# Performance work log

Hardware: AMD Instinct MI355X
Metric: run time of the kernel (lower is better)

Reference implementation:

```python
import jax, jax.numpy as jnp
import numpy as np

NUM_SEGMENTS = 16

def setup_inputs() -> dict:
    key = jax.random.key(0)
    k1, k2, k3, k4 = jax.random.split(key, 4)
    C, R = 256, 4
    x = jax.random.normal(k1, (1000000, C), dtype=jnp.float32)
    indices = jax.random.randint(k2, (1000000,), 0, NUM_SEGMENTS, dtype=jnp.int64)
    # Linear weights (torch Linear: y = x @ W.T); store as (in, out) for einsum
    w1 = jax.random.normal(k3, (C, C // R), dtype=jnp.float32) / np.sqrt(C)
    w2 = jax.random.normal(k4, (C // R, C), dtype=jnp.float32) / np.sqrt(C // R)
    return {"x": x, "indices": indices, "w1": w1, "w2": w2}

def reference(x, indices, w1, w2):
    idx = indices.astype(jnp.int32)
    # scatter-mean over segments: (S, C)
    seg_sum = jax.ops.segment_sum(x, idx, num_segments=NUM_SEGMENTS)
    counts = jax.ops.segment_sum(jnp.ones((x.shape[0],), x.dtype), idx, num_segments=NUM_SEGMENTS)
    seg_mean = seg_sum / jnp.maximum(counts, 1.0)[:, None]
    # tiny SE MLP: Linear -> ReLU -> Linear -> Sigmoid
    h = jax.nn.relu(seg_mean @ w1)
    gate = jax.nn.sigmoid(h @ w2)  # (S, C)
    # gather per-point gate and modulate
    return x * gate[idx]
```

## Files before the change

### kernel.cpp

```cpp
#include <hip/hip_runtime.h>
#include <math.h>

#define C 256
#define S 16
#define CR 64
#define NREP 8

__global__ __launch_bounds__(128) void k_segsum(
    const float* __restrict__ x, const int* __restrict__ idx,
    float* __restrict__ psum, int* __restrict__ pcnt, int nrows)
{
    __shared__ float ls[S][C];
    __shared__ int   lc[S];
    const int t = threadIdx.x;

    #pragma unroll
    for (int i = t; i < S * C; i += 128) (&ls[0][0])[i] = 0.0f;
    if (t < S) lc[t] = 0;
    __syncthreads();

    const float2* __restrict__ x2 = reinterpret_cast<const float2*>(x);
    for (int row = blockIdx.x; row < nrows; row += gridDim.x) {
        const int s = idx[row];
        float2 v = x2[row * (C / 2) + t];
        float2* p = reinterpret_cast<float2*>(&ls[s][2 * t]);
        float2 cur = *p;
        cur.x += v.x; cur.y += v.y;
        *p = cur;
        if (t == 0) lc[s]++;
    }
    __syncthreads();

    const int rep = blockIdx.x & (NREP - 1);
    float* gs = psum + rep * S * C;
    int*   gc = pcnt + rep * S;
    for (int i = t; i < S * C; i += 128) atomicAdd(&gs[i], (&ls[0][0])[i]);
    if (t < S) atomicAdd(&gc[t], lc[t]);
}

__global__ __launch_bounds__(256) void k_mlp(
    const float* __restrict__ psum, const int* __restrict__ pcnt,
    const float* __restrict__ w1, const float* __restrict__ w2,
    float* __restrict__ gate)
{
    __shared__ float sm[S][C];
    __shared__ float h[S][CR];
    __shared__ float cnt[S];
    const int t = threadIdx.x;

    if (t < S) {
        int c = 0;
        #pragma unroll
        for (int r = 0; r < NREP; r++) c += pcnt[r * S + t];
        cnt[t] = fmaxf((float)c, 1.0f);
    }
    __syncthreads();

    for (int i = t; i < S * C; i += 256) {
        float v = 0.0f;
        #pragma unroll
        for (int r = 0; r < NREP; r++) v += psum[r * S * C + i];
        sm[i / C][i % C] = v / cnt[i / C];
    }
    __syncthreads();

    for (int o = t; o < S * CR; o += 256) {
        const int s = o / CR, j = o % CR;
        float acc = 0.0f;
        #pragma unroll 4
        for (int k = 0; k < C; k++) acc += sm[s][k] * w1[k * CR + j];
        h[s][j] = fmaxf(acc, 0.0f);
    }
    __syncthreads();

    for (int o = t; o < S * C; o += 256) {
        const int s = o / C, j = o % C;
        float acc = 0.0f;
        #pragma unroll
        for (int k = 0; k < CR; k++) acc += h[s][k] * w2[k * C + j];
        gate[o] = 1.0f / (1.0f + expf(-acc));
    }
}

__global__ __launch_bounds__(256) void k_mod(
    const float* __restrict__ x, const int* __restrict__ idx,
    const float* __restrict__ gate, float* __restrict__ out, int nrows)
{
    const int l    = threadIdx.x & 63;
    const int wrow = threadIdx.x >> 6;
    const float4* __restrict__ x4 = reinterpret_cast<const float4*>(x);
    const float4* __restrict__ g4 = reinterpret_cast<const float4*>(gate);
    float4* __restrict__ o4 = reinterpret_cast<float4*>(out);

    for (int row = blockIdx.x * 4 + wrow; row < nrows; row += gridDim.x * 4) {
        const int s = idx[row];
        float4 v = x4[row * (C / 4) + l];
        const float4 g = g4[s * (C / 4) + l];
        v.x *= g.x; v.y *= g.y; v.z *= g.z; v.w *= g.w;
        o4[row * (C / 4) + l] = v;
    }
}

extern "C" void kernel_launch(void* const* d_in, const int* in_sizes, int n_in,
                              void* d_out, int out_size, void* d_ws, size_t ws_size,
                              hipStream_t stream)
{
    const float* x   = (const float*)d_in[0];
    const int*   idx = (const int*)  d_in[1];
    const float* w1  = (const float*)d_in[2];
    const float* w2  = (const float*)d_in[3];
    float* out = (float*)d_out;
    const int nrows = in_sizes[1];

    float* psum = (float*)d_ws;
    int*   pcnt = (int*)(psum + NREP * S * C);
    float* gate = (float*)(pcnt + NREP * S);

    const size_t zero_bytes = NREP * S * C * sizeof(float) + NREP * S * sizeof(int);
    hipMemsetAsync(d_ws, 0, zero_bytes, stream);

    k_segsum<<<2048, 128, 0, stream>>>(x, idx, psum, pcnt, nrows);
    k_mlp<<<1, 256, 0, stream>>>(psum, pcnt, w1, w2, gate);
    k_mod<<<2048, 256, 0, stream>>>(x, idx, gate, out, nrows);
}
```

Baseline: 768.5 us.

## Accumulate segment sums in per-wave registers with software prefetch

The segment-sum kernel now gives each 64-lane wave its own rows and keeps all 16 segment accumulators as float4 registers. A wave-uniform switch selects which accumulator a row goes into, replacing the shared-memory read-modify-write and the block-level syncs. Loads are double-buffered two rows ahead to hide memory latency, and the flush uses more replicas (NREP=16) to spread atomic contention. The modulate kernel processes two rows per iteration to raise memory-level parallelism. The cost is much higher register pressure (64+ accumulator VGPRs) and more global atomics at the end.

```diff
diff --git a/kernel.cpp b/kernel.cpp
--- a/kernel.cpp
+++ b/kernel.cpp
@@ -4,38 +4,67 @@
 #define C 256
 #define S 16
 #define CR 64
-#define NREP 8
+#define NREP 16
 
-__global__ __launch_bounds__(128) void k_segsum(
+__global__ __launch_bounds__(256) void k_segsum(
     const float* __restrict__ x, const int* __restrict__ idx,
     float* __restrict__ psum, int* __restrict__ pcnt, int nrows)
 {
-    __shared__ float ls[S][C];
-    __shared__ int   lc[S];
-    const int t = threadIdx.x;
+    const int lane = threadIdx.x & 63;
+    const int wid  = __builtin_amdgcn_readfirstlane(
+                        (blockIdx.x * blockDim.x + threadIdx.x) >> 6);
+    const int nw   = (gridDim.x * blockDim.x) >> 6;
 
-    #pragma unroll
-    for (int i = t; i < S * C; i += 128) (&ls[0][0])[i] = 0.0f;
-    if (t < S) lc[t] = 0;
-    __syncthreads();
+    float4 a0={0,0,0,0},a1={0,0,0,0},a2={0,0,0,0},a3={0,0,0,0},
+           a4={0,0,0,0},a5={0,0,0,0},a6={0,0,0,0},a7={0,0,0,0},
+           a8={0,0,0,0},a9={0,0,0,0},a10={0,0,0,0},a11={0,0,0,0},
+           a12={0,0,0,0},a13={0,0,0,0},a14={0,0,0,0},a15={0,0,0,0};
+    int c0=0,c1=0,c2=0,c3=0,c4=0,c5=0,c6=0,c7=0,
+        c8=0,c9=0,c10=0,c11=0,c12=0,c13=0,c14=0,c15=0;
 
-    const float2* __restrict__ x2 = reinterpret_cast<const float2*>(x);
-    for (int row = blockIdx.x; row < nrows; row += gridDim.x) {
-        const int s = idx[row];
-        float2 v = x2[row * (C / 2) + t];
-        float2* p = reinterpret_cast<float2*>(&ls[s][2 * t]);
-        float2 cur = *p;
-        cur.x += v.x; cur.y += v.y;
-        *p = cur;
-        if (t == 0) lc[s]++;
+    const float4* __restrict__ x4 = reinterpret_cast<const float4*>(x);
+
+    int   row = wid;
+    bool  p0 = row < nrows;
+    float4 v0 = {0,0,0,0}; int s0 = 0;
+    if (p0) { v0 = x4[row * (C/4) + lane]; s0 = idx[row]; }
+    int   rowN = row + nw;
+    bool  p1 = rowN < nrows;
+    float4 v1 = {0,0,0,0}; int s1 = 0;
+    if (p1) { v1 = x4[rowN * (C/4) + lane]; s1 = idx[rowN]; }
+
+    while (p0) {
+        const int rowP = rowN + nw;
+        const bool p2 = rowP < nrows;
+        float4 v2 = {0,0,0,0}; int s2 = 0;
+        if (p2) { v2 = x4[rowP * (C/4) + lane]; s2 = idx[rowP]; }
+
+        #define ACASE(K) case K: a##K.x+=v0.x; a##K.y+=v0.y; a##K.z+=v0.z; a##K.w+=v0.w; c##K++; break;
+        switch (__builtin_amdgcn_readfirstlane(s0)) {
+            ACASE(0)  ACASE(1)  ACASE(2)  ACASE(3)
+            ACASE(4)  ACASE(5)  ACASE(6)  ACASE(7)
+            ACASE(8)  ACASE(9)  ACASE(10) ACASE(11)
+            ACASE(12) ACASE(13) ACASE(14) ACASE(15)
+        }
+        #undef ACASE
+
+        v0 = v1; s0 = s1; p0 = p1;
+        v1 = v2; s1 = s2; p1 = p2;
+        rowN = rowP;
     }
-    __syncthreads();
 
-    const int rep = blockIdx.x & (NREP - 1);
+    const int rep = wid & (NREP - 1);
     float* gs = psum + rep * S * C;
     int*   gc = pcnt + rep * S;
-    for (int i = t; i < S * C; i += 128) atomicAdd(&gs[i], (&ls[0][0])[i]);
-    if (t < S) atomicAdd(&gc[t], lc[t]);
+    #define FLUSH(K) { float* p = gs + K * C + 4 * lane; \
+        atomicAdd(p + 0, a##K.x); atomicAdd(p + 1, a##K.y); \
+        atomicAdd(p + 2, a##K.z); atomicAdd(p + 3, a##K.w); \
+        if (lane == 0 && c##K) atomicAdd(&gc[K], c##K); }
+    FLUSH(0)  FLUSH(1)  FLUSH(2)  FLUSH(3)
+    FLUSH(4)  FLUSH(5)  FLUSH(6)  FLUSH(7)
+    FLUSH(8)  FLUSH(9)  FLUSH(10) FLUSH(11)
+    FLUSH(12) FLUSH(13) FLUSH(14) FLUSH(15)
+    #undef FLUSH
 }
 
 __global__ __launch_bounds__(256) void k_mlp(
@@ -86,18 +115,31 @@
     const float* __restrict__ x, const int* __restrict__ idx,
     const float* __restrict__ gate, float* __restrict__ out, int nrows)
 {
-    const int l    = threadIdx.x & 63;
-    const int wrow = threadIdx.x >> 6;
+    const int l  = threadIdx.x & 63;
+    const int w  = threadIdx.x >> 6;
+    const int gw = blockIdx.x * 4 + w;
+    const int nw = gridDim.x * 4;
     const float4* __restrict__ x4 = reinterpret_cast<const float4*>(x);
     const float4* __restrict__ g4 = reinterpret_cast<const float4*>(gate);
     float4* __restrict__ o4 = reinterpret_cast<float4*>(out);
 
-    for (int row = blockIdx.x * 4 + wrow; row < nrows; row += gridDim.x * 4) {
-        const int s = idx[row];
-        float4 v = x4[row * (C / 4) + l];
-        const float4 g = g4[s * (C / 4) + l];
-        v.x *= g.x; v.y *= g.y; v.z *= g.z; v.w *= g.w;
-        o4[row * (C / 4) + l] = v;
+    for (int row = gw; row < nrows; row += 2 * nw) {
+        const int r2 = row + nw;
+        const bool has2 = r2 < nrows;
+        const int sA = idx[row];
+        float4 vA = x4[row * (C/4) + l];
+        int sB = 0; float4 vB = {0,0,0,0};
+        if (has2) { sB = idx[r2]; vB = x4[r2 * (C/4) + l]; }
+
+        const float4 gA = g4[sA * (C/4) + l];
+        vA.x *= gA.x; vA.y *= gA.y; vA.z *= gA.z; vA.w *= gA.w;
+        o4[row * (C/4) + l] = vA;
+
+        if (has2) {
+            const float4 gB = g4[sB * (C/4) + l];
+            vB.x *= gB.x; vB.y *= gB.y; vB.z *= gB.z; vB.w *= gB.w;
+            o4[r2 * (C/4) + l] = vB;
+        }
     }
 }
 
@@ -119,7 +161,7 @@
     const size_t zero_bytes = NREP * S * C * sizeof(float) + NREP * S * sizeof(int);
     hipMemsetAsync(d_ws, 0, zero_bytes, stream);
 
-    k_segsum<<<2048, 128, 0, stream>>>(x, idx, psum, pcnt, nrows);
+    k_segsum<<<1024, 256, 0, stream>>>(x, idx, psum, pcnt, nrows);
     k_mlp<<<1, 256, 0, stream>>>(psum, pcnt, w1, w2, gate);
     k_mod<<<2048, 256, 0, stream>>>(x, idx, gate, out, nrows);
 }
```

Result: slower. 940.8 us (+22.4%).

## Accumulate segment sums in per-wave registers instead of shared memory

Applied to the files above, without the earlier changes.

Rewrites the segment-sum kernel so each 64-lane wave processes 64-row superblocks. It keeps 16 float4 per-segment accumulators in registers, selected via a readlane-uniform switch, and computes counts with ballot/popcount. This removes the shared-memory read-modify-write per row and the block barriers, and loads float4 per lane with 4-row unrolled loads. In exchange, every wave flushes 16×256 atomics to global memory (NREP raised to 16), which adds heavy register pressure and many more global atomics.

```diff
diff --git a/kernel.cpp b/kernel.cpp
--- a/kernel.cpp
+++ b/kernel.cpp
@@ -4,38 +4,84 @@
 #define C 256
 #define S 16
 #define CR 64
-#define NREP 8
+#define NREP 16
 
-__global__ __launch_bounds__(128) void k_segsum(
+__global__ __launch_bounds__(256) void k_segsum(
     const float* __restrict__ x, const int* __restrict__ idx,
     float* __restrict__ psum, int* __restrict__ pcnt, int nrows)
 {
-    __shared__ float ls[S][C];
-    __shared__ int   lc[S];
-    const int t = threadIdx.x;
+    const int lane = threadIdx.x & 63;
+    const int wid  = (blockIdx.x * blockDim.x + threadIdx.x) >> 6;
+    const int nw   = (gridDim.x * blockDim.x) >> 6;
 
-    #pragma unroll
-    for (int i = t; i < S * C; i += 128) (&ls[0][0])[i] = 0.0f;
-    if (t < S) lc[t] = 0;
-    __syncthreads();
+    float4 a0={0,0,0,0},a1={0,0,0,0},a2={0,0,0,0},a3={0,0,0,0},
+           a4={0,0,0,0},a5={0,0,0,0},a6={0,0,0,0},a7={0,0,0,0},
+           a8={0,0,0,0},a9={0,0,0,0},a10={0,0,0,0},a11={0,0,0,0},
+           a12={0,0,0,0},a13={0,0,0,0},a14={0,0,0,0},a15={0,0,0,0};
+    int c0=0,c1=0,c2=0,c3=0,c4=0,c5=0,c6=0,c7=0,
+        c8=0,c9=0,c10=0,c11=0,c12=0,c13=0,c14=0,c15=0;
 
-    const float2* __restrict__ x2 = reinterpret_cast<const float2*>(x);
-    for (int row = blockIdx.x; row < nrows; row += gridDim.x) {
-        const int s = idx[row];
-        float2 v = x2[row * (C / 2) + t];
-        float2* p = reinterpret_cast<float2*>(&ls[s][2 * t]);
-        float2 cur = *p;
-        cur.x += v.x; cur.y += v.y;
-        *p = cur;
-        if (t == 0) lc[s]++;
+    const float4* __restrict__ x4 = reinterpret_cast<const float4*>(x);
+    const int nsb = nrows >> 6;
+
+    #define SCASE(K, V) case K: a##K.x+=V.x; a##K.y+=V.y; a##K.z+=V.z; a##K.w+=V.w; break;
+    #define SW(sv, V) switch (sv) { \
+        SCASE(0,V)  SCASE(1,V)  SCASE(2,V)  SCASE(3,V) \
+        SCASE(4,V)  SCASE(5,V)  SCASE(6,V)  SCASE(7,V) \
+        SCASE(8,V)  SCASE(9,V)  SCASE(10,V) SCASE(11,V) \
+        SCASE(12,V) SCASE(13,V) SCASE(14,V) SCASE(15,V) }
+
+    for (int sb = wid; sb < nsb; sb += nw) {
+        const int row0 = sb << 6;
+        const int vidx = idx[row0 + lane];
+        #define CNT(K) c##K += (int)__popcll(__ballot(vidx == K));
+        CNT(0)  CNT(1)  CNT(2)  CNT(3)  CNT(4)  CNT(5)  CNT(6)  CNT(7)
+        CNT(8)  CNT(9)  CNT(10) CNT(11) CNT(12) CNT(13) CNT(14) CNT(15)
+        #undef CNT
+
+        const float4* __restrict__ p = x4 + (size_t)row0 * (C/4) + lane;
+        for (int j = 0; j < 64; j += 4) {
+            const float4 v0 = p[(j+0) * (C/4)];
+            const float4 v1 = p[(j+1) * (C/4)];
+            const float4 v2 = p[(j+2) * (C/4)];
+            const float4 v3 = p[(j+3) * (C/4)];
+            const int s0 = __builtin_amdgcn_readlane(vidx, j+0);
+            const int s1 = __builtin_amdgcn_readlane(vidx, j+1);
+            const int s2 = __builtin_amdgcn_readlane(vidx, j+2);
+            const int s3 = __builtin_amdgcn_readlane(vidx, j+3);
+            SW(s0, v0) SW(s1, v1) SW(s2, v2) SW(s3, v3)
+        }
     }
-    __syncthreads();
 
-    const int rep = blockIdx.x & (NREP - 1);
+    if (wid == 0) {
+        #define TCASE(K, V) case K: a##K.x+=V.x; a##K.y+=V.y; a##K.z+=V.z; a##K.w+=V.w; c##K++; break;
+        for (int row = nsb << 6; row < nrows; ++row) {
+            const int s = idx[row];
+            const float4 v = x4[(size_t)row * (C/4) + lane];
+            switch (s) {
+                TCASE(0,v)  TCASE(1,v)  TCASE(2,v)  TCASE(3,v)
+                TCASE(4,v)  TCASE(5,v)  TCASE(6,v)  TCASE(7,v)
+                TCASE(8,v)  TCASE(9,v)  TCASE(10,v) TCASE(11,v)
+                TCASE(12,v) TCASE(13,v) TCASE(14,v) TCASE(15,v)
+            }
+        }
+        #undef TCASE
+    }
+    #undef SW
+    #undef SCASE
+
+    const int rep = wid & (NREP - 1);
     float* gs = psum + rep * S * C;
     int*   gc = pcnt + rep * S;
-    for (int i = t; i < S * C; i += 128) atomicAdd(&gs[i], (&ls[0][0])[i]);
-    if (t < S) atomicAdd(&gc[t], lc[t]);
+    #define FLUSH(K) { float* fp = gs + K * C + 4 * lane; \
+        atomicAdd(fp + 0, a##K.x); atomicAdd(fp + 1, a##K.y); \
+        atomicAdd(fp + 2, a##K.z); atomicAdd(fp + 3, a##K.w); \
+        if (lane == 0 && c##K) atomicAdd(&gc[K], c##K); }
+    FLUSH(0)  FLUSH(1)  FLUSH(2)  FLUSH(3)
+    FLUSH(4)  FLUSH(5)  FLUSH(6)  FLUSH(7)
+    FLUSH(8)  FLUSH(9)  FLUSH(10) FLUSH(11)
+    FLUSH(12) FLUSH(13) FLUSH(14) FLUSH(15)
+    #undef FLUSH
 }
 
 __global__ __launch_bounds__(256) void k_mlp(
@@ -119,7 +165,7 @@
     const size_t zero_bytes = NREP * S * C * sizeof(float) + NREP * S * sizeof(int);
     hipMemsetAsync(d_ws, 0, zero_bytes, stream);
 
-    k_segsum<<<2048, 128, 0, stream>>>(x, idx, psum, pcnt, nrows);
+    k_segsum<<<2048, 256, 0, stream>>>(x, idx, psum, pcnt, nrows);
     k_mlp<<<1, 256, 0, stream>>>(psum, pcnt, w1, w2, gate);
     k_mod<<<2048, 256, 0, stream>>>(x, idx, gate, out, nrows);
 }
```

Result: slower. 1.155 ms (+50.3%).

## Accumulate segment sums in per-wave registers and split counts into ballot histogram kernel

Applied to the files above, without the earlier changes.

The segment-sum kernel now keeps all 16 segment accumulators in registers per wavefront. Each row is added to every accumulator through a 0/1 multiply mask, which replaces the LDS read-modify-write done per row. Segment counts move to a separate ballot/popcount histogram kernel, and the replica count rises to 16. The intent is to remove LDS latency and serialization in the streaming pass, which reads 1 GB of x. The cost is 16x redundant FMAs per element, heavy register use, and one extra kernel launch.

```diff
diff --git a/kernel.cpp b/kernel.cpp
--- a/kernel.cpp
+++ b/kernel.cpp
@@ -4,38 +4,99 @@
 #define C 256
 #define S 16
 #define CR 64
-#define NREP 8
+#define NREP 16
 
-__global__ __launch_bounds__(128) void k_segsum(
+__global__ __launch_bounds__(256) void k_hist(
+    const int* __restrict__ idx, int* __restrict__ pcnt, int nrows)
+{
+    const int lane = threadIdx.x & 63;
+    const int tid  = blockIdx.x * blockDim.x + threadIdx.x;
+    const int T    = gridDim.x * blockDim.x;
+    const int padded = ((nrows + 63) >> 6) << 6;
+
+    int c0=0,c1=0,c2=0,c3=0,c4=0,c5=0,c6=0,c7=0,
+        c8=0,c9=0,c10=0,c11=0,c12=0,c13=0,c14=0,c15=0;
+
+    for (int i = tid; i < padded; i += T) {
+        const int v = (i < nrows) ? idx[i] : -1;
+        #define CNT(K) c##K += (int)__popcll(__ballot(v == K));
+        CNT(0)  CNT(1)  CNT(2)  CNT(3)  CNT(4)  CNT(5)  CNT(6)  CNT(7)
+        CNT(8)  CNT(9)  CNT(10) CNT(11) CNT(12) CNT(13) CNT(14) CNT(15)
+        #undef CNT
+    }
+    if (lane == 0) {
+        #define FL(K) if (c##K) atomicAdd(&pcnt[K], c##K);
+        FL(0)  FL(1)  FL(2)  FL(3)  FL(4)  FL(5)  FL(6)  FL(7)
+        FL(8)  FL(9)  FL(10) FL(11) FL(12) FL(13) FL(14) FL(15)
+        #undef FL
+    }
+}
+
+__global__ __launch_bounds__(256, 2) void k_segsum(
     const float* __restrict__ x, const int* __restrict__ idx,
-    float* __restrict__ psum, int* __restrict__ pcnt, int nrows)
+    float* __restrict__ psum, int nrows)
 {
-    __shared__ float ls[S][C];
-    __shared__ int   lc[S];
-    const int t = threadIdx.x;
+    const int lane = threadIdx.x & 63;
+    const int w    = threadIdx.x >> 6;
+    const int gw   = blockIdx.x * 4 + w;
+    const int nw   = gridDim.x * 4;
 
-    #pragma unroll
-    for (int i = t; i < S * C; i += 128) (&ls[0][0])[i] = 0.0f;
-    if (t < S) lc[t] = 0;
+    float4 a0={0,0,0,0},a1={0,0,0,0},a2={0,0,0,0},a3={0,0,0,0},
+           a4={0,0,0,0},a5={0,0,0,0},a6={0,0,0,0},a7={0,0,0,0},
+           a8={0,0,0,0},a9={0,0,0,0},a10={0,0,0,0},a11={0,0,0,0},
+           a12={0,0,0,0},a13={0,0,0,0},a14={0,0,0,0},a15={0,0,0,0};
+
+    const float4* __restrict__ x4 = reinterpret_cast<const float4*>(x);
+
+    #define ACC1(K, sv, vv) { const float m = (sv == K) ? 1.0f : 0.0f; \
+        a##K.x = fmaf(m, vv.x, a##K.x); a##K.y = fmaf(m, vv.y, a##K.y); \
+        a##K.z = fmaf(m, vv.z, a##K.z); a##K.w = fmaf(m, vv.w, a##K.w); }
+    #define ROW(sv, vv) \
+        ACC1(0,sv,vv)  ACC1(1,sv,vv)  ACC1(2,sv,vv)  ACC1(3,sv,vv) \
+        ACC1(4,sv,vv)  ACC1(5,sv,vv)  ACC1(6,sv,vv)  ACC1(7,sv,vv) \
+        ACC1(8,sv,vv)  ACC1(9,sv,vv)  ACC1(10,sv,vv) ACC1(11,sv,vv) \
+        ACC1(12,sv,vv) ACC1(13,sv,vv) ACC1(14,sv,vv) ACC1(15,sv,vv)
+
+    const int nbatch = nrows >> 2;
+    for (int b = gw; b < nbatch; b += nw) {
+        const int r = b << 2;
+        const int s0 = __builtin_amdgcn_readfirstlane(idx[r + 0]);
+        const int s1 = __builtin_amdgcn_readfirstlane(idx[r + 1]);
+        const int s2 = __builtin_amdgcn_readfirstlane(idx[r + 2]);
+        const int s3 = __builtin_amdgcn_readfirstlane(idx[r + 3]);
+        const float4* __restrict__ p = x4 + (size_t)r * (C/4) + lane;
+        const float4 v0 = p[0 * (C/4)];
+        const float4 v1 = p[1 * (C/4)];
+        const float4 v2 = p[2 * (C/4)];
+        const float4 v3 = p[3 * (C/4)];
+        ROW(s0, v0) ROW(s1, v1) ROW(s2, v2) ROW(s3, v3)
+    }
+    if (gw == 0) {
+        for (int r = nbatch << 2; r < nrows; ++r) {
+            const int s = __builtin_amdgcn_readfirstlane(idx[r]);
+            const float4 v = x4[(size_t)r * (C/4) + lane];
+            ROW(s, v)
+        }
+    }
+    #undef ROW
+    #undef ACC1
+
+    __shared__ float red[4][S][C];
+    #define ST(K) *reinterpret_cast<float4*>(&red[w][K][4 * lane]) = a##K;
+    ST(0)  ST(1)  ST(2)  ST(3)  ST(4)  ST(5)  ST(6)  ST(7)
+    ST(8)  ST(9)  ST(10) ST(11) ST(12) ST(13) ST(14) ST(15)
+    #undef ST
     __syncthreads();
 
-    const float2* __restrict__ x2 = reinterpret_cast<const float2*>(x);
-    for (int row = blockIdx.x; row < nrows; row += gridDim.x) {
-        const int s = idx[row];
-        float2 v = x2[row * (C / 2) + t];
-        float2* p = reinterpret_cast<float2*>(&ls[s][2 * t]);
-        float2 cur = *p;
-        cur.x += v.x; cur.y += v.y;
-        *p = cur;
-        if (t == 0) lc[s]++;
+    const int t   = threadIdx.x;
+    const int rep = blockIdx.x & (NREP - 1);
+    float* gs = psum + (size_t)rep * S * C;
+    #pragma unroll
+    for (int s_ = 0; s_ < S; s_++) {
+        const float v = red[0][s_][t] + red[1][s_][t] +
+                        red[2][s_][t] + red[3][s_][t];
+        atomicAdd(&gs[s_ * C + t], v);
     }
-    __syncthreads();
-
-    const int rep = blockIdx.x & (NREP - 1);
-    float* gs = psum + rep * S * C;
-    int*   gc = pcnt + rep * S;
-    for (int i = t; i < S * C; i += 128) atomicAdd(&gs[i], (&ls[0][0])[i]);
-    if (t < S) atomicAdd(&gc[t], lc[t]);
 }
 
 __global__ __launch_bounds__(256) void k_mlp(
@@ -48,12 +109,7 @@
     __shared__ float cnt[S];
     const int t = threadIdx.x;
 
-    if (t < S) {
-        int c = 0;
-        #pragma unroll
-        for (int r = 0; r < NREP; r++) c += pcnt[r * S + t];
-        cnt[t] = fmaxf((float)c, 1.0f);
-    }
+    if (t < S) cnt[t] = fmaxf((float)pcnt[t], 1.0f);
     __syncthreads();
 
     for (int i = t; i < S * C; i += 256) {
@@ -114,12 +170,13 @@
 
     float* psum = (float*)d_ws;
     int*   pcnt = (int*)(psum + NREP * S * C);
-    float* gate = (float*)(pcnt + NREP * S);
+    float* gate = (float*)(pcnt + S);
 
-    const size_t zero_bytes = NREP * S * C * sizeof(float) + NREP * S * sizeof(int);
+    const size_t zero_bytes = NREP * S * C * sizeof(float) + S * sizeof(int);
     hipMemsetAsync(d_ws, 0, zero_bytes, stream);
 
-    k_segsum<<<2048, 128, 0, stream>>>(x, idx, psum, pcnt, nrows);
-    k_mlp<<<1, 256, 0, stream>>>(psum, pcnt, w1, w2, gate);
-    k_mod<<<2048, 256, 0, stream>>>(x, idx, gate, out, nrows);
+    k_hist  <<<  64, 256, 0, stream>>>(idx, pcnt, nrows);
+    k_segsum<<<1024, 256, 0, stream>>>(x, idx, psum, nrows);
+    k_mlp   <<<   1, 256, 0, stream>>>(psum, pcnt, w1, w2, gate);
+    k_mod   <<<2048, 256, 0, stream>>>(x, idx, gate, out, nrows);
 }
```

After: 740.2 us. 3.7% less time.
